# Kernel optimization log

Hardware: AMD Instinct MI355X
Metric: run time of the kernel (lower is better)

The kernel has to match this reference:

```python
import jax, jax.numpy as jnp
import numpy as np

B, NM, T, RED = 8, 10, 16376, 8
D, H, L = 512, 8, 4
DH = D // H
BS, NG, NW, NR = 64, 1, 3, 2
S = T // RED + 1          # 2048 tokens incl. CLS
NB = S // BS              # 32 blocks
FF = 2048


def _ln(x, g, b):
    m = x.mean(-1, keepdims=True)
    v = ((x - m) ** 2).mean(-1, keepdims=True)
    return (x - m) / jnp.sqrt(v + 1e-5) * g + b


def setup_inputs() -> dict:
    key = jax.random.key(0)
    ks = jax.random.split(key, 16)
    p = lambda k, sh: jax.random.normal(k, sh, jnp.float32) * 0.02
    return {
        "x": jax.random.normal(ks[0], (B, NM, T), jnp.float32),
        "w_embed": p(ks[1], (NM * RED, D)), "b_embed": jnp.zeros((D,), jnp.float32),
        "pos_emb": p(ks[2], (S, D)),
        "Wq": p(ks[3], (L, D, D)), "bq": jnp.zeros((L, D), jnp.float32),
        "Wk": p(ks[4], (L, D, D)), "bk": jnp.zeros((L, D), jnp.float32),
        "Wv": p(ks[5], (L, D, D)), "bv": jnp.zeros((L, D), jnp.float32),
        "Wo": p(ks[6], (L, D, D)), "bo": jnp.zeros((L, D), jnp.float32),
        "ln1_g": jnp.ones((L, D), jnp.float32), "ln1_b": jnp.zeros((L, D), jnp.float32),
        "W1": p(ks[7], (L, D, FF)), "b1": jnp.zeros((L, FF), jnp.float32),
        "W2": p(ks[8], (L, FF, D)), "b2": jnp.zeros((L, D), jnp.float32),
        "ln2_g": jnp.ones((L, D), jnp.float32), "ln2_b": jnp.zeros((L, D), jnp.float32),
        "w_dense": p(ks[9], (D, 1024)), "b_dense": jnp.zeros((1024,), jnp.float32),
        "w_out": p(ks[10], (1024, 2)), "b_out": jnp.zeros((2,), jnp.float32),
        "rand_blocks": jax.random.randint(ks[11], (NB, NR), 0, NB),
    }


def _fwd(x, w_embed, b_embed, pos_emb, Wq, bq, Wk, bk, Wv, bv, Wo, bo,
         ln1_g, ln1_b, W1, b1, W2, b2, ln2_g, ln2_b,
         w_dense, b_dense, w_out, b_out, rand_blocks):
    Bx = x.shape[0]
    # [B, NM, T] -> view [B, NM*RED, T//RED] -> transpose -> [B, S-1, NM*RED]
    h = x.reshape(Bx, NM * RED, -1).transpose(0, 2, 1)
    h = h @ w_embed + b_embed
    cls = jnp.zeros((Bx, 1, D), h.dtype)
    h = jnp.concatenate([cls, h], axis=1) + pos_emb[None]  # learned pos-enc

    # block-sparse context: static global + window blocks, dynamic random blocks
    win = np.clip(np.arange(NB)[:, None] + np.arange(NW)[None, :] - NW // 2, 0, NB - 1)
    glb = np.broadcast_to(np.arange(NG)[None, :], (NB, NG))
    idx = jnp.concatenate([jnp.asarray(np.concatenate([glb, win], 1)), rand_blocks], axis=1)  # [NB, C]
    C = idx.shape[1]
    # mask context blocks that duplicate an earlier block for the same query block
    dup = jnp.tril(idx[:, :, None] == idx[:, None, :], -1).any(-1)  # [NB, C]
    scale = 1.0 / np.sqrt(DH)

    for l in range(L):
        def heads(w, b):
            return (h @ w + b).reshape(Bx, S, H, DH).transpose(0, 2, 1, 3).reshape(Bx, H, NB, BS, DH)
        q, k, v = heads(Wq[l], bq[l]), heads(Wk[l], bk[l]), heads(Wv[l], bv[l])
        kg, vg = k[:, :, idx], v[:, :, idx]             # [B, H, NB, C, BS, DH] block gather
        sc = jnp.einsum('bhnqd,bhncsd->bhnqcs', q, kg) * scale
        sc = jnp.where(dup[None, None, :, None, :, None], -1e9, sc)
        attn = jax.nn.softmax(sc.reshape(Bx, H, NB, BS, C * BS), axis=-1).reshape(sc.shape)
        o = jnp.einsum('bhnqcs,bhncsd->bhnqd', attn, vg)
        o = o.reshape(Bx, H, S, DH).transpose(0, 2, 1, 3).reshape(Bx, S, D) @ Wo[l] + bo[l]
        h = _ln(h + o, ln1_g[l], ln1_b[l])
        ff = jax.nn.relu(h @ W1[l] + b1[l]) @ W2[l] + b2[l]
        h = _ln(h + ff, ln2_g[l], ln2_b[l])

    dense = jax.nn.relu(h[:, 0] @ w_dense + b_dense)  # CLS readout
    return jnp.tanh(dense @ w_out + b_out)            # [B, 2]


def reference(x, w_embed, b_embed, pos_emb, Wq, bq, Wk, bk, Wv, bv, Wo, bo,
              ln1_g, ln1_b, W1, b1, W2, b2, ln2_g, ln2_b,
              w_dense, b_dense, w_out, b_out, rand_blocks):
    return _fwd(x, w_embed, b_embed, pos_emb, Wq, bq, Wk, bk, Wv, bv, Wo, bo,
                ln1_g, ln1_b, W1, b1, W2, b2, ln2_g, ln2_b,
                w_dense, b_dense, w_out, b_out, rand_blocks)
```

## Files before the change

### kernel.cpp

```cpp
#include <hip/hip_runtime.h>
#include <cstdint>
#include <cstddef>

#define B_   8
#define NM_  10
#define T_   16376
#define D_   512
#define H_   8
#define DH_  64
#define L_   4
#define S_   2048
#define NB_  32
#define BS_  64
#define FF_  2048
#define MTOK (B_*S_)
#define DD_  (D_*D_)
#define KE_  128

typedef __attribute__((ext_vector_type(8))) __bf16 bf16x8;
typedef __attribute__((ext_vector_type(4))) __bf16 bf16x4;
typedef __attribute__((ext_vector_type(4))) float f32x4;

__device__ __forceinline__ void async16(void* lds, const void* g) {
    __builtin_amdgcn_global_load_lds(
        (const __attribute__((address_space(1))) void*)g,
        (__attribute__((address_space(3))) void*)lds, 16, 0, 0);
}

#define SWZ64(row, kq) (((row) << 3) + ((kq) ^ ((row) & 7)))

__global__ __launch_bounds__(256) void wconv_kernel(
    const float* __restrict__ in, __bf16* __restrict__ outp, int K, int N, int Kp)
{
    __shared__ float t[32][33];
    const float* ip = in + (size_t)blockIdx.z * K * N;
    __bf16* op = outp + (size_t)blockIdx.z * N * Kp;
    int n0 = blockIdx.x * 32, k0 = blockIdx.y * 32;
    int tx = threadIdx.x, ty = threadIdx.y;
    #pragma unroll
    for (int j = 0; j < 4; j++) {
        int k = k0 + ty + 8 * j;
        t[ty + 8 * j][tx] = (k < K) ? ip[(size_t)k * N + n0 + tx] : 0.f;
    }
    __syncthreads();
    #pragma unroll
    for (int j = 0; j < 4; j++)
        op[(size_t)(n0 + ty + 8 * j) * Kp + k0 + tx] = (__bf16)t[tx][ty + 8 * j];
}

__global__ __launch_bounds__(256) void wconv_qkvo(
    const float* __restrict__ wq, const float* __restrict__ wk,
    const float* __restrict__ wv, const float* __restrict__ wo,
    __bf16* __restrict__ wtqkv, __bf16* __restrict__ wto)
{
    __shared__ float t[32][33];
    int zz = blockIdx.z;
    int mat = zz >> 2, layer = zz & 3;
    const float* src = (mat == 0 ? wq : mat == 1 ? wk : mat == 2 ? wv : wo)
                       + (size_t)layer * DD_;
    __bf16* dst = (mat < 3) ? wtqkv + ((size_t)mat * L_ + layer) * DD_
                            : wto + (size_t)layer * DD_;
    int n0 = blockIdx.x * 32, k0 = blockIdx.y * 32;
    int tx = threadIdx.x, ty = threadIdx.y;
    #pragma unroll
    for (int j = 0; j < 4; j++)
        t[ty + 8 * j][tx] = src[(size_t)(k0 + ty + 8 * j) * D_ + n0 + tx];
    __syncthreads();
    #pragma unroll
    for (int j = 0; j < 4; j++)
        dst[(size_t)(n0 + ty + 8 * j) * D_ + k0 + tx] = (__bf16)t[tx][ty + 8 * j];
}

__global__ __launch_bounds__(256) void xbuild_kernel(
    const float* __restrict__ x, __bf16* __restrict__ xr)
{
    __shared__ float xs[64][KE_ + 1];
    int row0 = blockIdx.x * 64;
    int b = row0 >> 11;
    int t0 = row0 & (S_ - 1);
    int tid = threadIdx.x;
    int lane = tid & 63;
    int mq = tid >> 6;
    for (int mb = 0; mb < 32; mb++) {
        int m = mb * 4 + mq;
        int t = t0 + lane;
        float v = 0.f;
        if (m < 80 && t > 0)
            v = x[(size_t)b * NM_ * T_ + (size_t)(m >> 3) * T_ + (m & 7) * 2047 + (t - 1)];
        xs[lane][m] = v;
    }
    __syncthreads();
    #pragma unroll
    for (int u = 0; u < 8; u++) {
        int ch = tid + u * 256;
        int row = ch >> 5, c4 = (ch & 31) * 4;
        bf16x4 pk;
        #pragma unroll
        for (int i = 0; i < 4; i++) pk[i] = (__bf16)xs[row][c4 + i];
        *(bf16x4*)&xr[(size_t)(row0 + row) * KE_ + c4] = pk;
    }
}

__global__ __launch_bounds__(256, 2) void mfma_gemm(
    const __bf16* __restrict__ A, const __bf16* __restrict__ Wt,
    const float* __restrict__ bias0, const float* __restrict__ bias1,
    const float* __restrict__ bias2,
    const float* __restrict__ pe, float* __restrict__ Cf, __bf16* __restrict__ Cb,
    int N, int K, long wtz, long cbz, int relu, int scatter, int nz)
{
    __shared__ __align__(16) __bf16 As[2][128 * 64];
    __shared__ __align__(16) __bf16 Bs[2][128 * 64];
    int tid = threadIdx.x;
    int wave = tid >> 6;
    int lane = tid & 63;

    int nbx = gridDim.x, nby = gridDim.y;
    int bxIdx, bmIdx;
    if ((nby & 7) == 0) {
        int id = blockIdx.y * nbx + blockIdx.x;
        int chunk = nby >> 3;
        int xcd = id & 7;
        int local = id >> 3;
        int row = local / nbx;
        bmIdx = xcd * chunk + row;
        bxIdx = local - row * nbx;
    } else {
        bxIdx = blockIdx.x; bmIdx = blockIdx.y;
    }
    int z = bxIdx % nz;
    int bn = (bxIdx / nz) * 128;
    int bm = bmIdx * 128;
    const __bf16* Wz = Wt + (size_t)z * wtz;
    const float* bias = (z == 0) ? bias0 : (z == 1 ? bias1 : bias2);

    f32x4 acc[4][4];
    #pragma unroll
    for (int r = 0; r < 4; r++)
        #pragma unroll
        for (int c = 0; c < 4; c++) acc[r][c] = (f32x4){0.f, 0.f, 0.f, 0.f};

    const int wr = (wave >> 1) * 64;
    const int wc = (wave & 1) * 64;
    const int fr = lane & 15;
    const int kqi = lane >> 4;

    const __bf16* pA[4];
    const __bf16* pB[4];
    int ldsoff[4];
    #pragma unroll
    for (int u = 0; u < 4; u++) {
        int p = tid + 256 * u;
        int row = p >> 3;
        int kq = (p & 7) ^ (row & 7);
        pA[u] = A  + (size_t)(bm + row) * K + kq * 8;
        pB[u] = Wz + (size_t)(bn + row) * K + kq * 8;
        ldsoff[u] = (u * 256 + wave * 64) * 8;
    }

    __bf16 *a_cur = As[0], *a_nxt = As[1];
    __bf16 *b_cur = Bs[0], *b_nxt = Bs[1];

    #pragma unroll
    for (int u = 0; u < 4; u++) {
        async16(a_cur + ldsoff[u], pA[u]);
        async16(b_cur + ldsoff[u], pB[u]);
    }

    for (int kk = 0; kk < K; kk += 64) {
        __syncthreads();
        if (kk + 64 < K) {
            #pragma unroll
            for (int u = 0; u < 4; u++) {
                async16(a_nxt + ldsoff[u], pA[u] + kk + 64);
                async16(b_nxt + ldsoff[u], pB[u] + kk + 64);
            }
        }
        #pragma unroll
        for (int ks = 0; ks < 2; ks++) {
            int kq0 = ks * 4 + kqi;
            bf16x8 af[4], bfr[4];
            #pragma unroll
            for (int r = 0; r < 4; r++)
                af[r] = *(const bf16x8*)&a_cur[SWZ64(wr + r * 16 + fr, kq0) * 8];
            #pragma unroll
            for (int c = 0; c < 4; c++)
                bfr[c] = *(const bf16x8*)&b_cur[SWZ64(wc + c * 16 + fr, kq0) * 8];
            #pragma unroll
            for (int r = 0; r < 4; r++)
                #pragma unroll
                for (int c = 0; c < 4; c++)
                    acc[r][c] = __builtin_amdgcn_mfma_f32_16x16x32_bf16(af[r], bfr[c], acc[r][c], 0, 0, 0);
        }
        __bf16* t;
        t = a_cur; a_cur = a_nxt; a_nxt = t;
        t = b_cur; b_cur = b_nxt; b_nxt = t;
    }

    int rbase = bm + wr + (lane >> 4) * 4;
    #pragma unroll
    for (int c = 0; c < 4; c++) {
        int cg = bn + wc + c * 16 + fr;
        float bv = bias[cg];
        #pragma unroll
        for (int r = 0; r < 4; r++) {
            int rg0 = rbase + r * 16;
            float vals[4];
            #pragma unroll
            for (int i = 0; i < 4; i++) {
                float val = acc[r][c][i] + bv;
                if (relu) val = fmaxf(val, 0.f);
                if (pe) {
                    int t = (rg0 + i) & (S_ - 1);
                    val = (t == 0) ? pe[cg] : val + pe[(size_t)t * N + cg];
                }
                vals[i] = val;
            }
            if (Cf) {
                #pragma unroll
                for (int i = 0; i < 4; i++) Cf[(size_t)(rg0 + i) * N + cg] = vals[i];
            }
            if (Cb) {
                if (scatter) {
                    int bb = rg0 >> 11;
                    int s0 = rg0 & (S_ - 1);
                    int hh = cg >> 6, dh = cg & 63;
                    if (z == 2) {
                        bf16x4 pk;
                        #pragma unroll
                        for (int i = 0; i < 4; i++) pk[i] = (__bf16)vals[i];
                        *(bf16x4*)(Cb + (size_t)z * cbz +
                                   ((((size_t)bb * H_ + hh) * DH_ + dh) * S_) + s0) = pk;
                    } else {
                        #pragma unroll
                        for (int i = 0; i < 4; i++)
                            (Cb + (size_t)z * cbz)[((((size_t)bb * H_ + hh) * S_ + s0 + i) * DH_) + dh] = (__bf16)vals[i];
                    }
                } else {
                    #pragma unroll
                    for (int i = 0; i < 4; i++) Cb[(size_t)(rg0 + i) * N + cg] = (__bf16)vals[i];
                }
            }
        }
    }
}

#define KSTR 72
__global__ __launch_bounds__(256, 4) void attn_kernel(
    const __bf16* __restrict__ q, const __bf16* __restrict__ k,
    const __bf16* __restrict__ vt, const int* __restrict__ rb,
    __bf16* __restrict__ o)
{
    __shared__ __align__(16) __bf16 Ks[64 * KSTR];
    __shared__ __align__(16) __bf16 Vs[64 * KSTR];
    __shared__ __align__(16) __bf16 Ps[64 * KSTR];
    int bid = blockIdx.x;
    int xcd = bid & 7;
    int local = bid >> 3;
    int bh = (local >> 5) * 8 + xcd;
    int n = local & 31;
    int b = bh >> 3;
    int hh = bh & 7;
    int tid = threadIdx.x;
    int wave = tid >> 6;
    int lane = tid & 63;
    const int fr = lane & 15;
    const int fq = lane >> 4;

    int idx[6];
    idx[0] = 0;
    idx[1] = n > 0 ? n - 1 : 0;
    idx[2] = n;
    idx[3] = n < NB_ - 1 ? n + 1 : NB_ - 1;
    idx[4] = rb[n * 2 + 0];
    idx[5] = rb[n * 2 + 1];

    const size_t plane = ((size_t)b * H_ + hh) * S_;
    const __bf16* vtb = vt + plane * DH_;

    const __bf16* qrow = q + (plane + (size_t)n * BS_ + wave * 16 + fr) * DH_ + fq * 8;
    bf16x8 qf0 = *(const bf16x8*)qrow;
    bf16x8 qf1 = *(const bf16x8*)(qrow + 32);

    f32x4 oacc[4];
    #pragma unroll
    for (int dt = 0; dt < 4; dt++) oacc[dt] = (f32x4){0.f, 0.f, 0.f, 0.f};
    float mrow = -1e30f, lrow = 0.f;

    for (int c = 0; c < 6; c++) {
        bool dup = false;
        #pragma unroll
        for (int j = 0; j < 6; j++) if (j < c && idx[j] == idx[c]) dup = true;
        if (dup) continue;

        __syncthreads();
        {
            const __bf16* kb = k + (plane + (size_t)idx[c] * BS_) * DH_;
            const __bf16* vb = vtb + (size_t)idx[c] * BS_;
            #pragma unroll
            for (int u = 0; u < 2; u++) {
                int ch = tid + u * 256;
                int row = ch >> 3, d0 = (ch & 7) * 8;
                *(bf16x8*)&Ks[row * KSTR + d0] = *(const bf16x8*)(kb + row * DH_ + d0);
                *(bf16x8*)&Vs[row * KSTR + d0] = *(const bf16x8*)(vb + (size_t)row * S_ + d0);
            }
        }
        __syncthreads();

        f32x4 st[4];
        #pragma unroll
        for (int t = 0; t < 4; t++) {
            bf16x8 ka0 = *(const bf16x8*)&Ks[(t * 16 + fr) * KSTR + fq * 8];
            bf16x8 ka1 = *(const bf16x8*)&Ks[(t * 16 + fr) * KSTR + 32 + fq * 8];
            st[t] = __builtin_amdgcn_mfma_f32_16x16x32_bf16(ka0, qf0, (f32x4){0.f,0.f,0.f,0.f}, 0, 0, 0);
            st[t] = __builtin_amdgcn_mfma_f32_16x16x32_bf16(ka1, qf1, st[t], 0, 0, 0);
        }
        float rmax = -1e30f;
        #pragma unroll
        for (int t = 0; t < 4; t++)
            #pragma unroll
            for (int i = 0; i < 4; i++) {
                st[t][i] *= 0.125f;
                rmax = fmaxf(rmax, st[t][i]);
            }
        rmax = fmaxf(rmax, __shfl_xor(rmax, 16));
        rmax = fmaxf(rmax, __shfl_xor(rmax, 32));
        float newm = fmaxf(mrow, rmax);
        float corr = __expf(mrow - newm);
        mrow = newm;
        float psum = 0.f;
        #pragma unroll
        for (int t = 0; t < 4; t++) {
            bf16x4 pk;
            #pragma unroll
            for (int i = 0; i < 4; i++) {
                float p = __expf(st[t][i] - newm);
                psum += p;
                pk[i] = (__bf16)p;
            }
            *(bf16x4*)&Ps[(wave * 16 + fr) * KSTR + t * 16 + fq * 4] = pk;
        }
        psum += __shfl_xor(psum, 16);
        psum += __shfl_xor(psum, 32);
        lrow = lrow * corr + psum;

        #pragma unroll
        for (int i = 0; i < 4; i++) {
            float ci = __shfl(corr, fq * 4 + i);
            #pragma unroll
            for (int dt = 0; dt < 4; dt++) oacc[dt][i] *= ci;
        }

        bf16x8 pa0 = *(const bf16x8*)&Ps[(wave * 16 + fr) * KSTR + fq * 8];
        bf16x8 pa1 = *(const bf16x8*)&Ps[(wave * 16 + fr) * KSTR + 32 + fq * 8];
        #pragma unroll
        for (int dt = 0; dt < 4; dt++) {
            bf16x8 vb0 = *(const bf16x8*)&Vs[(dt * 16 + fr) * KSTR + fq * 8];
            bf16x8 vb1 = *(const bf16x8*)&Vs[(dt * 16 + fr) * KSTR + 32 + fq * 8];
            oacc[dt] = __builtin_amdgcn_mfma_f32_16x16x32_bf16(pa0, vb0, oacc[dt], 0, 0, 0);
            oacc[dt] = __builtin_amdgcn_mfma_f32_16x16x32_bf16(pa1, vb1, oacc[dt], 0, 0, 0);
        }
    }

    float linv = 1.f / lrow;
    #pragma unroll
    for (int i = 0; i < 4; i++) {
        float li = __shfl(linv, fq * 4 + i);
        int s = n * BS_ + wave * 16 + fq * 4 + i;
        __bf16* op = o + ((size_t)b * S_ + s) * D_ + hh * DH_ + fr;
        #pragma unroll
        for (int dt = 0; dt < 4; dt++)
            op[dt * 16] = (__bf16)(oacc[dt][i] * li);
    }
}

__global__ __launch_bounds__(256) void ln_add_kernel(
    float* h, const __bf16* __restrict__ delta, __bf16* __restrict__ hb,
    const float* __restrict__ g, const float* __restrict__ bb)
{
    size_t r = (size_t)blockIdx.x * 4 + (threadIdx.x >> 6);
    int t = threadIdx.x & 63;
    float4* hp = (float4*)(h + r * D_) + 2 * t;
    float4 x0 = hp[0], x1 = hp[1];
    bf16x8 dv = *(const bf16x8*)&delta[r * D_ + t * 8];
    float x[8] = {x0.x, x0.y, x0.z, x0.w, x1.x, x1.y, x1.z, x1.w};
    #pragma unroll
    for (int j = 0; j < 8; j++) x[j] += (float)dv[j];
    float s = 0.f;
    #pragma unroll
    for (int j = 0; j < 8; j++) s += x[j];
    #pragma unroll
    for (int off = 32; off; off >>= 1) s += __shfl_xor(s, off, 64);
    float mean = s * (1.0f / D_);
    float ss = 0.f;
    #pragma unroll
    for (int j = 0; j < 8; j++) { x[j] -= mean; ss += x[j] * x[j]; }
    #pragma unroll
    for (int off = 32; off; off >>= 1) ss += __shfl_xor(ss, off, 64);
    float rs = rsqrtf(ss * (1.0f / D_) + 1e-5f);
    float4 g0 = ((const float4*)g)[2 * t], g1 = ((const float4*)g)[2 * t + 1];
    float4 b0 = ((const float4*)bb)[2 * t], b1 = ((const float4*)bb)[2 * t + 1];
    float gg[8] = {g0.x, g0.y, g0.z, g0.w, g1.x, g1.y, g1.z, g1.w};
    float bbv[8] = {b0.x, b0.y, b0.z, b0.w, b1.x, b1.y, b1.z, b1.w};
    float y[8];
    bf16x8 outv;
    #pragma unroll
    for (int j = 0; j < 8; j++) {
        y[j] = x[j] * rs * gg[j] + bbv[j];
        outv[j] = (__bf16)y[j];
    }
    hp[0] = (float4){y[0], y[1], y[2], y[3]};
    hp[1] = (float4){y[4], y[5], y[6], y[7]};
    *(bf16x8*)&hb[r * D_ + t * 8] = outv;
}

__global__ __launch_bounds__(256) void head1_kernel(
    const float* __restrict__ h, const float* __restrict__ wd,
    const float* __restrict__ bd, const float* __restrict__ wo,
    float* __restrict__ partial)
{
    __shared__ float hrow[D_];
    __shared__ float red[8];
    int b = blockIdx.x, jg = blockIdx.y;
    int tid = threadIdx.x;
    if (tid < 128) ((float4*)hrow)[tid] = ((const float4*)(h + (size_t)b * S_ * D_))[tid];
    __syncthreads();
    int j = jg * 256 + tid;
    float acc = bd[j];
    #pragma unroll 8
    for (int i = 0; i < D_; i++) acc = fmaf(hrow[i], wd[(size_t)i * 1024 + j], acc);
    float dns = fmaxf(acc, 0.f);
    float2 w2 = ((const float2*)wo)[j];
    float p0 = dns * w2.x, p1 = dns * w2.y;
    #pragma unroll
    for (int off = 32; off; off >>= 1) { p0 += __shfl_xor(p0, off, 64); p1 += __shfl_xor(p1, off, 64); }
    int wid = tid >> 6;
    if ((tid & 63) == 0) { red[wid * 2] = p0; red[wid * 2 + 1] = p1; }
    __syncthreads();
    if (tid == 0) {
        float t0 = red[0] + red[2] + red[4] + red[6];
        float t1 = red[1] + red[3] + red[5] + red[7];
        partial[((size_t)b * 4 + jg) * 2 + 0] = t0;
        partial[((size_t)b * 4 + jg) * 2 + 1] = t1;
    }
}

__global__ __launch_bounds__(64) void head2_kernel(
    const float* __restrict__ partial, const float* __restrict__ bo,
    float* __restrict__ out)
{
    int tid = threadIdx.x;
    if (tid < 16) {
        int b = tid >> 1, c = tid & 1;
        float s = bo[c];
        #pragma unroll
        for (int jg = 0; jg < 4; jg++) s += partial[((size_t)b * 4 + jg) * 2 + c];
        out[b * 2 + c] = tanhf(s);
    }
}

extern "C" void kernel_launch(void* const* d_in, const int* in_sizes, int n_in,
                              void* d_out, int out_size, void* d_ws, size_t ws_size,
                              hipStream_t stream) {
    (void)in_sizes; (void)n_in; (void)out_size; (void)ws_size;
    const float* x       = (const float*)d_in[0];
    const float* w_embed = (const float*)d_in[1];
    const float* b_embed = (const float*)d_in[2];
    const float* pos_emb = (const float*)d_in[3];
    const float* Wq      = (const float*)d_in[4];
    const float* bq      = (const float*)d_in[5];
    const float* Wk      = (const float*)d_in[6];
    const float* bk      = (const float*)d_in[7];
    const float* Wv      = (const float*)d_in[8];
    const float* bv      = (const float*)d_in[9];
    const float* Wo      = (const float*)d_in[10];
    const float* bo      = (const float*)d_in[11];
    const float* ln1_g   = (const float*)d_in[12];
    const float* ln1_b   = (const float*)d_in[13];
    const float* W1      = (const float*)d_in[14];
    const float* b1      = (const float*)d_in[15];
    const float* W2      = (const float*)d_in[16];
    const float* b2      = (const float*)d_in[17];
    const float* ln2_g   = (const float*)d_in[18];
    const float* ln2_b   = (const float*)d_in[19];
    const float* w_dense = (const float*)d_in[20];
    const float* b_dense = (const float*)d_in[21];
    const float* w_out   = (const float*)d_in[22];
    const float* b_out   = (const float*)d_in[23];
    const int*   rb      = (const int*)d_in[24];
    float* out = (float*)d_out;

    const size_t PLANE = (size_t)B_ * H_ * S_ * DH_;
    float*  h    = (float*)d_ws;
    __bf16* h_bf = (__bf16*)((char*)d_ws + (size_t)32 * 1024 * 1024);
    __bf16* big  = (__bf16*)((char*)d_ws + (size_t)48 * 1024 * 1024);
    __bf16* qkv  = big;
    __bf16* o_bf = big + 3 * PLANE;
    __bf16* ff1  = big;
    __bf16* xr   = big;
    __bf16* wt_e = big + (size_t)28 * 1024 * 1024;
    __bf16* wt   = (__bf16*)((char*)d_ws + (size_t)112 * 1024 * 1024);
    __bf16* wt_qkv = wt;
    __bf16* wt_o   = wt_qkv + (size_t)3 * L_ * DD_;
    __bf16* wt_1   = wt_o + (size_t)L_ * DD_;
    __bf16* wt_2   = wt_1 + (size_t)L_ * D_ * FF_;
    __bf16* dbuf   = (__bf16*)((char*)d_ws + (size_t)138 * 1024 * 1024);
    float*  hpart  = (float*)((char*)d_ws + (size_t)154 * 1024 * 1024);

    dim3 tb(32, 8);
    wconv_qkvo<<<dim3(16, 16, 16), tb, 0, stream>>>(Wq, Wk, Wv, Wo, wt_qkv, wt_o);
    wconv_kernel<<<dim3(64, 16, L_), tb, 0, stream>>>(W1, wt_1, D_, FF_, D_);
    wconv_kernel<<<dim3(16, 64, L_), tb, 0, stream>>>(W2, wt_2, FF_, D_, FF_);
    wconv_kernel<<<dim3(16, 4, 1),  tb, 0, stream>>>(w_embed, wt_e, 80, D_, KE_);

    xbuild_kernel<<<MTOK / 64, 256, 0, stream>>>(x, xr);
    mfma_gemm<<<dim3(D_ / 128, MTOK / 128, 1), 256, 0, stream>>>(
        xr, wt_e, b_embed, b_embed, b_embed,
        pos_emb, h, h_bf, D_, KE_, 0, 0, 0, 0, 1);

    for (int l = 0; l < L_; l++) {
        mfma_gemm<<<dim3((D_ / 128) * 3, MTOK / 128, 1), 256, 0, stream>>>(
            h_bf, wt_qkv + (size_t)l * DD_, bq + l * D_, bk + l * D_, bv + l * D_,
            nullptr, nullptr, qkv, D_, D_, (long)L_ * DD_, (long)PLANE, 0, 1, 3);

        attn_kernel<<<B_ * H_ * NB_, 256, 0, stream>>>(qkv, qkv + PLANE, qkv + 2 * PLANE, rb, o_bf);

        mfma_gemm<<<dim3(D_ / 128, MTOK / 128, 1), 256, 0, stream>>>(
            o_bf, wt_o + (size_t)l * DD_, bo + l * D_, bo + l * D_, bo + l * D_,
            nullptr, nullptr, dbuf, D_, D_, 0, 0, 0, 0, 1);
        ln_add_kernel<<<MTOK / 4, 256, 0, stream>>>(h, dbuf, h_bf, ln1_g + l * D_, ln1_b + l * D_);

        mfma_gemm<<<dim3(FF_ / 128, MTOK / 128, 1), 256, 0, stream>>>(
            h_bf, wt_1 + (size_t)l * D_ * FF_, b1 + l * FF_, b1 + l * FF_, b1 + l * FF_,
            nullptr, nullptr, ff1, FF_, D_, 0, 0, 1, 0, 1);

        mfma_gemm<<<dim3(D_ / 128, MTOK / 128, 1), 256, 0, stream>>>(
            ff1, wt_2 + (size_t)l * FF_ * D_, b2 + l * D_, b2 + l * D_, b2 + l * D_,
            nullptr, nullptr, dbuf, D_, FF_, 0, 0, 0, 0, 1);
        ln_add_kernel<<<MTOK / 4, 256, 0, stream>>>(h, dbuf, h_bf, ln2_g + l * D_, ln2_b + l * D_);
    }

    head1_kernel<<<dim3(B_, 4), 256, 0, stream>>>(h, w_dense, b_dense, w_out, hpart);
    head2_kernel<<<1, 64, 0, stream>>>(hpart, b_out, out);
}
```

Measured before the change: 1.095 ms.

## Enlarge GEMM tile to 256x128 with 512 threads and triple-buffered LDS pipeline

The MFMA GEMM now uses 8 waves per block and computes a 256x128 output tile instead of 128x128, which halves the number of M-blocks and improves reuse of the B tile. The LDS pipeline goes from double to triple buffering. It uses explicit vmcnt waits and s_barrier so that two k-stages of global-to-LDS loads stay in flight, and it raises wave priority around the MFMA burst. The cost is about 144KB of LDS per block, which allows only one block per CU, and fewer blocks in the grid to spread across CUs.

```diff
diff --git a/kernel.cpp b/kernel.cpp
--- a/kernel.cpp
+++ b/kernel.cpp
@@ -101,15 +101,15 @@
     }
 }
 
-__global__ __launch_bounds__(256, 2) void mfma_gemm(
+__global__ __launch_bounds__(512, 2) void mfma_gemm(
     const __bf16* __restrict__ A, const __bf16* __restrict__ Wt,
     const float* __restrict__ bias0, const float* __restrict__ bias1,
     const float* __restrict__ bias2,
     const float* __restrict__ pe, float* __restrict__ Cf, __bf16* __restrict__ Cb,
     int N, int K, long wtz, long cbz, int relu, int scatter, int nz)
 {
-    __shared__ __align__(16) __bf16 As[2][128 * 64];
-    __shared__ __align__(16) __bf16 Bs[2][128 * 64];
+    __shared__ __align__(16) __bf16 As[3 * 256 * 64];
+    __shared__ __align__(16) __bf16 Bs[3 * 128 * 64];
     int tid = threadIdx.x;
     int wave = tid >> 6;
     int lane = tid & 63;
@@ -129,7 +129,7 @@
     }
     int z = bxIdx % nz;
     int bn = (bxIdx / nz) * 128;
-    int bm = bmIdx * 128;
+    int bm = bmIdx * 256;
     const __bf16* Wz = Wt + (size_t)z * wtz;
     const float* bias = (z == 0) ? bias0 : (z == 1 ? bias1 : bias2);
 
@@ -145,35 +145,47 @@
     const int kqi = lane >> 4;
 
     const __bf16* pA[4];
-    const __bf16* pB[4];
-    int ldsoff[4];
+    const __bf16* pB[2];
+    int ldsA[4], ldsB[2];
     #pragma unroll
     for (int u = 0; u < 4; u++) {
-        int p = tid + 256 * u;
+        int p = tid + 512 * u;
         int row = p >> 3;
         int kq = (p & 7) ^ (row & 7);
-        pA[u] = A  + (size_t)(bm + row) * K + kq * 8;
+        pA[u] = A + (size_t)(bm + row) * K + kq * 8;
+        ldsA[u] = (u * 512 + wave * 64) * 8;
+    }
+    #pragma unroll
+    for (int u = 0; u < 2; u++) {
+        int p = tid + 512 * u;
+        int row = p >> 3;
+        int kq = (p & 7) ^ (row & 7);
         pB[u] = Wz + (size_t)(bn + row) * K + kq * 8;
-        ldsoff[u] = (u * 256 + wave * 64) * 8;
-    }
-
-    __bf16 *a_cur = As[0], *a_nxt = As[1];
-    __bf16 *b_cur = Bs[0], *b_nxt = Bs[1];
-
-    #pragma unroll
-    for (int u = 0; u < 4; u++) {
-        async16(a_cur + ldsoff[u], pA[u]);
-        async16(b_cur + ldsoff[u], pB[u]);
-    }
-
-    for (int kk = 0; kk < K; kk += 64) {
-        __syncthreads();
-        if (kk + 64 < K) {
-            #pragma unroll
-            for (int u = 0; u < 4; u++) {
-                async16(a_nxt + ldsoff[u], pA[u] + kk + 64);
-                async16(b_nxt + ldsoff[u], pB[u] + kk + 64);
-            }
+        ldsB[u] = (u * 512 + wave * 64) * 8;
+    }
+
+    __bf16 *a0 = As, *a1 = As + 256 * 64, *a2 = As + 2 * 256 * 64;
+    __bf16 *b0 = Bs, *b1 = Bs + 128 * 64, *b2 = Bs + 2 * 128 * 64;
+
+    #pragma unroll
+    for (int u = 0; u < 4; u++) async16(a0 + ldsA[u], pA[u]);
+    #pragma unroll
+    for (int u = 0; u < 2; u++) async16(b0 + ldsB[u], pB[u]);
+    asm volatile("" ::: "memory");
+    #pragma unroll
+    for (int u = 0; u < 4; u++) async16(a1 + ldsA[u], pA[u] + 64);
+    #pragma unroll
+    for (int u = 0; u < 2; u++) async16(b1 + ldsB[u], pB[u] + 64);
+    asm volatile("s_waitcnt vmcnt(6)\n\ts_barrier" ::: "memory");
+
+    const int NT = K >> 6;
+    for (int t = 0; t < NT; ++t) {
+        if (t + 2 < NT) {
+            int kk = (t + 2) * 64;
+            #pragma unroll
+            for (int u = 0; u < 4; u++) async16(a2 + ldsA[u], pA[u] + kk);
+            #pragma unroll
+            for (int u = 0; u < 2; u++) async16(b2 + ldsB[u], pB[u] + kk);
         }
         #pragma unroll
         for (int ks = 0; ks < 2; ks++) {
@@ -181,19 +193,22 @@
             bf16x8 af[4], bfr[4];
             #pragma unroll
             for (int r = 0; r < 4; r++)
-                af[r] = *(const bf16x8*)&a_cur[SWZ64(wr + r * 16 + fr, kq0) * 8];
+                af[r] = *(const bf16x8*)&a0[SWZ64(wr + r * 16 + fr, kq0) * 8];
             #pragma unroll
             for (int c = 0; c < 4; c++)
-                bfr[c] = *(const bf16x8*)&b_cur[SWZ64(wc + c * 16 + fr, kq0) * 8];
+                bfr[c] = *(const bf16x8*)&b0[SWZ64(wc + c * 16 + fr, kq0) * 8];
+            __builtin_amdgcn_s_setprio(1);
             #pragma unroll
             for (int r = 0; r < 4; r++)
                 #pragma unroll
                 for (int c = 0; c < 4; c++)
                     acc[r][c] = __builtin_amdgcn_mfma_f32_16x16x32_bf16(af[r], bfr[c], acc[r][c], 0, 0, 0);
-        }
-        __bf16* t;
-        t = a_cur; a_cur = a_nxt; a_nxt = t;
-        t = b_cur; b_cur = b_nxt; b_nxt = t;
+            __builtin_amdgcn_s_setprio(0);
+        }
+        if (t + 2 < NT) asm volatile("s_waitcnt vmcnt(6)\n\ts_barrier" ::: "memory");
+        else            asm volatile("s_waitcnt vmcnt(0)\n\ts_barrier" ::: "memory");
+        __bf16* ta = a0; a0 = a1; a1 = a2; a2 = ta;
+        __bf16* tb = b0; b0 = b1; b1 = b2; b2 = tb;
     }
 
     int rbase = bm + wr + (lane >> 4) * 4;
@@ -513,27 +528,27 @@
     wconv_kernel<<<dim3(16, 4, 1),  tb, 0, stream>>>(w_embed, wt_e, 80, D_, KE_);
 
     xbuild_kernel<<<MTOK / 64, 256, 0, stream>>>(x, xr);
-    mfma_gemm<<<dim3(D_ / 128, MTOK / 128, 1), 256, 0, stream>>>(
+    mfma_gemm<<<dim3(D_ / 128, MTOK / 256, 1), 512, 0, stream>>>(
         xr, wt_e, b_embed, b_embed, b_embed,
         pos_emb, h, h_bf, D_, KE_, 0, 0, 0, 0, 1);
 
     for (int l = 0; l < L_; l++) {
-        mfma_gemm<<<dim3((D_ / 128) * 3, MTOK / 128, 1), 256, 0, stream>>>(
+        mfma_gemm<<<dim3((D_ / 128) * 3, MTOK / 256, 1), 512, 0, stream>>>(
             h_bf, wt_qkv + (size_t)l * DD_, bq + l * D_, bk + l * D_, bv + l * D_,
             nullptr, nullptr, qkv, D_, D_, (long)L_ * DD_, (long)PLANE, 0, 1, 3);
 
         attn_kernel<<<B_ * H_ * NB_, 256, 0, stream>>>(qkv, qkv + PLANE, qkv + 2 * PLANE, rb, o_bf);
 
-        mfma_gemm<<<dim3(D_ / 128, MTOK / 128, 1), 256, 0, stream>>>(
+        mfma_gemm<<<dim3(D_ / 128, MTOK / 256, 1), 512, 0, stream>>>(
             o_bf, wt_o + (size_t)l * DD_, bo + l * D_, bo + l * D_, bo + l * D_,
             nullptr, nullptr, dbuf, D_, D_, 0, 0, 0, 0, 1);
         ln_add_kernel<<<MTOK / 4, 256, 0, stream>>>(h, dbuf, h_bf, ln1_g + l * D_, ln1_b + l * D_);
 
-        mfma_gemm<<<dim3(FF_ / 128, MTOK / 128, 1), 256, 0, stream>>>(
+        mfma_gemm<<<dim3(FF_ / 128, MTOK / 256, 1), 512, 0, stream>>>(
             h_bf, wt_1 + (size_t)l * D_ * FF_, b1 + l * FF_, b1 + l * FF_, b1 + l * FF_,
             nullptr, nullptr, ff1, FF_, D_, 0, 0, 1, 0, 1);
 
-        mfma_gemm<<<dim3(D_ / 128, MTOK / 128, 1), 256, 0, stream>>>(
+        mfma_gemm<<<dim3(D_ / 128, MTOK / 256, 1), 512, 0, stream>>>(
             ff1, wt_2 + (size_t)l * FF_ * D_, b2 + l * D_, b2 + l * D_, b2 + l * D_,
             nullptr, nullptr, dbuf, D_, FF_, 0, 0, 0, 0, 1);
         ln_add_kernel<<<MTOK / 4, 256, 0, stream>>>(h, dbuf, h_bf, ln2_g + l * D_, ln2_b + l * D_);
```

Result: slower. 1.217 ms (+11.2%).
